# Performance work log

Measured on AMD Instinct MI355X. Metric: run time of the kernel, lower is better.

The kernel has to match this reference:

```python
import jax, jax.numpy as jnp
import numpy as np

N = 8192
NUM_CLASSES = 81            # background + 80 fg classes (COCO)
SCORE_THRESH = 0.05
NMS_THRESH = 0.5
NUM_DETECTIONS = 100
REG_W = (10.0, 10.0, 5.0, 5.0)
MIN_SIZE = 1.0
BBOX_XFORM_CLIP = float(np.log(1000.0 / 16.0))


def setup_inputs() -> dict:
    key = jax.random.key(0)
    k1, k2, k3, k4 = jax.random.split(key, 4)
    xy1 = jax.random.uniform(k1, (N, 2), minval=0.0, maxval=700.0)
    wh = jax.random.uniform(k2, (N, 2), minval=8.0, maxval=300.0)
    proposal = jnp.concatenate([xy1, xy1 + wh], axis=1)          # [N,4] xyxy
    class_logit = jax.random.normal(k3, (N, NUM_CLASSES), dtype=jnp.float32)
    box_regression = jax.random.normal(k4, (N, NUM_CLASSES * 4), dtype=jnp.float32) * 0.5
    return {"proposal": proposal, "class_logit": class_logit,
            "box_regression": box_regression, "image_h": 800, "image_w": 1216}


def _decode(deltas, boxes):
    # deltas [..., N, 4] (per-class), boxes [N, 4] xyxy; standard Fast R-CNN BoxCoder.decode
    wx, wy, ww, wh = REG_W
    widths = boxes[:, 2] - boxes[:, 0]
    heights = boxes[:, 3] - boxes[:, 1]
    cx = boxes[:, 0] + 0.5 * widths
    cy = boxes[:, 1] + 0.5 * heights
    dx = deltas[..., 0] / wx
    dy = deltas[..., 1] / wy
    dw = jnp.minimum(deltas[..., 2] / ww, BBOX_XFORM_CLIP)
    dh = jnp.minimum(deltas[..., 3] / wh, BBOX_XFORM_CLIP)
    pcx = dx * widths + cx
    pcy = dy * heights + cy
    pw = jnp.exp(dw) * widths
    ph = jnp.exp(dh) * heights
    return jnp.stack([pcx - 0.5 * pw, pcy - 0.5 * ph,
                      pcx + 0.5 * pw, pcy + 0.5 * ph], axis=-1)


def _iou_one(box, boxes):
    # IoU of one box [4] against all boxes [N,4]
    lt = jnp.maximum(box[:2], boxes[:, :2])
    rb = jnp.minimum(box[2:], boxes[:, 2:])
    whc = jnp.clip(rb - lt, 0.0)
    inter = whc[:, 0] * whc[:, 1]
    a1 = (box[2] - box[0]) * (box[3] - box[1])
    a2 = (boxes[:, 2] - boxes[:, 0]) * (boxes[:, 3] - boxes[:, 1])
    return inter / (a1 + a2 - inter + 1e-12)


def _nms_per_class(boxes, scores):
    # Sequential greedy NMS: pick highest score, suppress IoU>thresh, repeat.
    # boxes [N,4], scores [N] (already 0 where filtered). Returns top NUM_DETECTIONS.
    def step(scores_w, _):
        j = jnp.argmax(scores_w)
        s = scores_w[j]
        valid = s > 0.0
        bj = boxes[j]
        iou = _iou_one(bj, boxes)                         # [N]
        new = jnp.where(iou > NMS_THRESH, 0.0, scores_w).at[j].set(0.0)
        new = jnp.where(valid, new, scores_w)
        return new, (bj, s, valid)
    _, (sel_b, sel_s, sel_v) = jax.lax.scan(step, scores, None, length=NUM_DETECTIONS)
    return sel_b, sel_s, sel_v                            # [D,4], [D], [D]


def reference(proposal, class_logit, box_regression, image_h, image_w):
    pred_score = jax.nn.softmax(class_logit, axis=-1)     # [N, C]
    deltas = box_regression.reshape(N, NUM_CLASSES, 4)
    fg_deltas = jnp.transpose(deltas[:, 1:, :], (1, 0, 2))  # [C-1, N, 4]
    boxes = _decode(fg_deltas, proposal)                    # [C-1, N, 4]
    # clip to image (process_box)
    W = jnp.float32(image_w); H = jnp.float32(image_h)
    x1 = jnp.clip(boxes[..., 0], 0.0, W)
    y1 = jnp.clip(boxes[..., 1], 0.0, H)
    x2 = jnp.clip(boxes[..., 2], 0.0, W)
    y2 = jnp.clip(boxes[..., 3], 0.0, H)
    boxes = jnp.stack([x1, y1, x2, y2], axis=-1)            # [C-1, N, 4]
    keep_size = ((x2 - x1) >= MIN_SIZE) & ((y2 - y1) >= MIN_SIZE)
    scores = jnp.transpose(pred_score[:, 1:])               # [C-1, N]
    scores = jnp.where((scores >= SCORE_THRESH) & keep_size, scores, 0.0)
    sel_b, sel_s, sel_v = jax.vmap(_nms_per_class)(boxes, scores)  # [C-1,D,...]
    out_boxes = sel_b.reshape(-1, 4)                         # [(C-1)*D, 4]
    out_scores = sel_s.reshape(-1)
    out_labels = jnp.repeat(jnp.arange(1, NUM_CLASSES, dtype=jnp.int32), NUM_DETECTIONS)
    out_valid = sel_v.reshape(-1)
    return out_boxes, out_scores, out_labels, out_valid
```

## Files before the change

kernel.cpp:

```cpp
#include <hip/hip_runtime.h>
#include <hip/hip_bf16.h>

#define NN 8192
#define NC 81
#define FG 80
#define ND 100
#define SH 8
#define CAPS 128
#define CPADI 32
#define MAXK 384
#define KW6 6
#define KROW 9
#define BBOX_CLIP 4.135166556742356f

__global__ __launch_bounds__(256) void decode_kernel(
    const float* __restrict__ prop,
    const float* __restrict__ logit,
    const float* __restrict__ reg,
    const int* __restrict__ ih, const int* __restrict__ iw,
    int* __restrict__ counts,
    float* __restrict__ boxes0,
    float* __restrict__ cbox,
    float* __restrict__ cscore)
{
    const int n = blockIdx.x * 4 + (threadIdx.x >> 6);
    const int shard = blockIdx.x & (SH - 1);
    const int lane = threadIdx.x & 63;
    const float* lrow = logit + (long)n * NC;

    float v1 = lrow[lane];
    float v2 = (lane < NC - 64) ? lrow[64 + lane] : -1e30f;
    float m = fmaxf(v1, v2);
#pragma unroll
    for (int off = 32; off; off >>= 1) m = fmaxf(m, __shfl_xor(m, off));
    float e = expf(v1 - m) + ((lane < NC - 64) ? expf(v2 - m) : 0.0f);
#pragma unroll
    for (int off = 32; off; off >>= 1) e += __shfl_xor(e, off);

    const float W = (float)iw[0];
    const float H = (float)ih[0];
    const float4 p = *(const float4*)(prop + n * 4);
    const float pw = p.z - p.x, ph = p.w - p.y;
    const float pcx = p.x + 0.5f * pw, pcy = p.y + 0.5f * ph;

    for (int c = 1 + lane; c <= FG; c += 64) {
        float score = expf(lrow[c] - m) / e;
        const float4 d = *(const float4*)(reg + (long)n * (NC * 4) + c * 4);
        float dx = d.x / 10.0f;
        float dy = d.y / 10.0f;
        float dw = fminf(d.z / 5.0f, BBOX_CLIP);
        float dh = fminf(d.w / 5.0f, BBOX_CLIP);
        float ncx = dx * pw + pcx;
        float ncy = dy * ph + pcy;
        float nw = expf(dw) * pw;
        float nh = expf(dh) * ph;
        float bx1 = ncx - 0.5f * nw, by1 = ncy - 0.5f * nh;
        float bx2 = ncx + 0.5f * nw, by2 = ncy + 0.5f * nh;
        bx1 = fminf(fmaxf(bx1, 0.0f), W);
        by1 = fminf(fmaxf(by1, 0.0f), H);
        bx2 = fminf(fmaxf(bx2, 0.0f), W);
        by2 = fminf(fmaxf(by2, 0.0f), H);
        bool keep = ((bx2 - bx1) >= 1.0f) && ((by2 - by1) >= 1.0f);

        if (n == 0) {
            float* b0 = boxes0 + (c - 1) * 4;
            b0[0] = bx1; b0[1] = by1; b0[2] = bx2; b0[3] = by2;
        }
        if (score >= 0.05f && keep) {
            const int slot = (c - 1) * SH + shard;
            int pos = atomicAdd(&counts[slot * CPADI], 1);
            if (pos < CAPS) {
                float* cb = cbox + ((long)slot * CAPS + pos) * 4;
                cb[0] = bx1; cb[1] = by1; cb[2] = bx2; cb[3] = by2;
                cscore[slot * CAPS + pos] = score;
            }
        }
    }
}

__global__ __launch_bounds__(1024) void nms_kernel(
    const int* __restrict__ counts,
    const float* __restrict__ boxes0,
    const float* __restrict__ cbox,
    const float* __restrict__ cscore,
    float* __restrict__ out)
{
    __shared__ __align__(16) float  s_sc[MAXK];
    __shared__ float4 s_ubox[MAXK];
    __shared__ int    s_sidx[MAXK];
    __shared__ float4 s_box[MAXK];
    __shared__ float  s_ss[MAXK];
    __shared__ unsigned long long s_row[MAXK * KROW];

    const int c = blockIdx.x;
    const int t = threadIdx.x;
    const int lane = t & 63;
    const int wv = t >> 6;

    int cnt0 = min(counts[(c * SH + 0) * CPADI], CAPS);
    int cnt1 = min(counts[(c * SH + 1) * CPADI], CAPS);
    int cnt2 = min(counts[(c * SH + 2) * CPADI], CAPS);
    int cnt3 = min(counts[(c * SH + 3) * CPADI], CAPS);
    int cnt4 = min(counts[(c * SH + 4) * CPADI], CAPS);
    int cnt5 = min(counts[(c * SH + 5) * CPADI], CAPS);
    int cnt6 = min(counts[(c * SH + 6) * CPADI], CAPS);
    int cnt7 = min(counts[(c * SH + 7) * CPADI], CAPS);
    int K = cnt0 + cnt1 + cnt2 + cnt3 + cnt4 + cnt5 + cnt6 + cnt7;
    if (K > MAXK) K = MAXK;
    const int KW = (K + 63) >> 6;


    for (int i = K + t; i < MAXK; i += 1024) {
        s_sc[i] = 0.0f;
        s_ss[i] = 0.0f;
        s_box[i] = make_float4(0.f, 0.f, 0.f, 0.f);
    }
    {
        const int s = t >> 7;
        const int i = t & (CAPS - 1);
        int mycnt = cnt0;
        if (s == 1) mycnt = cnt1; if (s == 2) mycnt = cnt2;
        if (s == 3) mycnt = cnt3; if (s == 4) mycnt = cnt4;
        if (s == 5) mycnt = cnt5; if (s == 6) mycnt = cnt6;
        if (s == 7) mycnt = cnt7;
        int offs = 0;
        if (s > 0) offs += cnt0; if (s > 1) offs += cnt1;
        if (s > 2) offs += cnt2; if (s > 3) offs += cnt3;
        if (s > 4) offs += cnt4; if (s > 5) offs += cnt5;
        if (s > 6) offs += cnt6;
        if (i < mycnt) {
            int d = offs + i;
            if (d < MAXK) {
                const long src = (long)(c * SH + s) * CAPS + i;
                s_sc[d] = cscore[src];
                s_ubox[d] = *(const float4*)(cbox + src * 4);
            }
        }
    }
    __syncthreads();

    if (t < K) {
        const float si = s_sc[t];
        const float4* s4 = (const float4*)s_sc;
        const int nch = (K + 3) >> 2;
        int r = 0;
        for (int ch = 0; ch < nch; ++ch) {
            const float4 sj = s4[ch];
            const int j = ch * 4;
            r += (sj.x > si) || (sj.x == si && (j + 0) < t);
            r += (sj.y > si) || (sj.y == si && (j + 1) < t);
            r += (sj.z > si) || (sj.z == si && (j + 2) < t);
            r += (sj.w > si) || (sj.w == si && (j + 3) < t);
        }
        s_sidx[r] = t;
    }
    __syncthreads();

    if (t < K) {
        const int i = s_sidx[t];
        s_box[t] = s_ubox[i];
        s_ss[t] = s_sc[i];
    }
    __syncthreads();

    float4 colb[KW6];
    float a2c[KW6];
#pragma unroll
    for (int w = 0; w < KW6; ++w) {
        const float4 b = s_box[w * 64 + lane];
        colb[w] = b;
        a2c[w] = (b.z - b.x) * (b.w - b.y);
    }

    for (int r = wv; r < K; r += 16) {
        const float4 rb = s_box[r];
        const float a1 = (rb.z - rb.x) * (rb.w - rb.y);
#pragma unroll
        for (int w = 0; w < KW6; ++w) {
            if (w < KW) {
                const float lx = fmaxf(rb.x, colb[w].x);
                const float ly = fmaxf(rb.y, colb[w].y);
                const float rx = fminf(rb.z, colb[w].z);
                const float ry = fminf(rb.w, colb[w].w);
                const float cw = fmaxf(rx - lx, 0.0f);
                const float ch = fmaxf(ry - ly, 0.0f);
                const float inter = cw * ch;
                const float iou = inter / (a1 + a2c[w] - inter + 1e-12f);
                const unsigned long long msk = __ballot(iou > 0.5f);
                if (lane == 0) s_row[r * KROW + w] = msk;
            }
        }
    }
    __syncthreads();

    if (wv != 0) return;

#define INIW(W) ((K >= (W)*64 + 64) ? ~0ull : ((K <= (W)*64) ? 0ull : ((~0ull) >> (64 - (K - (W)*64)))))
    const unsigned long long va0 = INIW(0), va1 = INIW(1), va2 = INIW(2);
    const unsigned long long va3 = INIW(3), va4 = INIW(4), va5 = INIW(5);
#undef INIW

    const unsigned long long ltm = (1ull << lane) - 1ull;

    unsigned long long v0 = va0, v1 = va1, v2 = va2;
    unsigned long long v3 = va3, v4 = va4, v5 = va5;

    for (int it = 0; it < MAXK; ++it) {
        unsigned long long nv0, nv1, nv2, nv3, nv4, nv5;
        {
            const unsigned long long* rp = s_row + (unsigned)(0 * 64 + lane) * KROW;
            unsigned long long s = rp[0] & v0 & ltm;
            nv0 = __ballot(s == 0ull) & va0;
        }
        {
            const unsigned long long* rp = s_row + (unsigned)(1 * 64 + lane) * KROW;
            unsigned long long s = (rp[0] & v0) | (rp[1] & v1 & ltm);
            nv1 = __ballot(s == 0ull) & va1;
        }
        {
            const unsigned long long* rp = s_row + (unsigned)(2 * 64 + lane) * KROW;
            unsigned long long s = (rp[0] & v0) | (rp[1] & v1) | (rp[2] & v2 & ltm);
            nv2 = __ballot(s == 0ull) & va2;
        }
        {
            const unsigned long long* rp = s_row + (unsigned)(3 * 64 + lane) * KROW;
            unsigned long long s = (rp[0] & v0) | (rp[1] & v1) | (rp[2] & v2) |
                                   (rp[3] & v3 & ltm);
            nv3 = __ballot(s == 0ull) & va3;
        }
        {
            const unsigned long long* rp = s_row + (unsigned)(4 * 64 + lane) * KROW;
            unsigned long long s = (rp[0] & v0) | (rp[1] & v1) | (rp[2] & v2) |
                                   (rp[3] & v3) | (rp[4] & v4 & ltm);
            nv4 = __ballot(s == 0ull) & va4;
        }
        {
            const unsigned long long* rp = s_row + (unsigned)(5 * 64 + lane) * KROW;
            unsigned long long s = (rp[0] & v0) | (rp[1] & v1) | (rp[2] & v2) |
                                   (rp[3] & v3) | (rp[4] & v4) | (rp[5] & v5 & ltm);
            nv5 = __ballot(s == 0ull) & va5;
        }
        const unsigned long long diff = (nv0 ^ v0) | (nv1 ^ v1) | (nv2 ^ v2) |
                                        (nv3 ^ v3) | (nv4 ^ v4) | (nv5 ^ v5);
        v0 = nv0; v1 = nv1; v2 = nv2; v3 = nv3; v4 = nv4; v5 = nv5;
        if (diff == 0ull) break;
    }

    float* ob = out + (long)c * ND * 4;
    float* os = out + (long)FG * ND * 4 + c * ND;
    float* ol = os + FG * ND;
    float* ov = ol + FG * ND;
    const float lab = (float)(c + 1);

    const int p0 = __popcll(v0), p1 = __popcll(v1), p2 = __popcll(v2);
    const int p3 = __popcll(v3), p4 = __popcll(v4);
    const int total = p0 + p1 + p2 + p3 + p4 + __popcll(v5);
    const int kept = total < ND ? total : ND;

    const float b0x1 = boxes0[c * 4 + 0], b0y1 = boxes0[c * 4 + 1];
    const float b0x2 = boxes0[c * 4 + 2], b0y2 = boxes0[c * 4 + 3];

    for (int d = lane; d < ND; d += 64) {
        if (d < kept) {
            int rr = d;
            unsigned long long x;
            int wbase;
            if (rr < p0) { x = v0; wbase = 0; }
            else { rr -= p0;
                if (rr < p1) { x = v1; wbase = 64; }
                else { rr -= p1;
                    if (rr < p2) { x = v2; wbase = 128; }
                    else { rr -= p2;
                        if (rr < p3) { x = v3; wbase = 192; }
                        else { rr -= p3;
                            if (rr < p4) { x = v4; wbase = 256; }
                            else { rr -= p4; x = v5; wbase = 320; }
                        }
                    }
                }
            }
            for (int k = 0; k < rr; ++k) x &= x - 1ull;
            const int i_d = wbase + __builtin_ctzll(x);
            const float4 kb = s_box[i_d];
            *(float4*)(ob + d * 4) = kb;
            os[d] = s_ss[i_d]; ol[d] = lab; ov[d] = 1.0f;
        } else {
            *(float4*)(ob + d * 4) = make_float4(b0x1, b0y1, b0x2, b0y2);
            os[d] = 0.0f; ol[d] = lab; ov[d] = 0.0f;
        }
    }
}

extern "C" void kernel_launch(void* const* d_in, const int* in_sizes, int n_in,
                              void* d_out, int out_size, void* d_ws, size_t ws_size,
                              hipStream_t stream) {
    const float* prop  = (const float*)d_in[0];
    const float* logit = (const float*)d_in[1];
    const float* reg   = (const float*)d_in[2];
    const int*   ih    = (const int*)d_in[3];
    const int*   iw    = (const int*)d_in[4];
    float* out = (float*)d_out;

    char* ws = (char*)d_ws;
    int*   counts = (int*)ws;
    float* boxes0 = (float*)(ws + 81920);
    float* cscore = (float*)(ws + 90112);
    float* cbox   = (float*)(ws + 90112 + (size_t)FG * SH * CAPS * 4);

    hipMemsetAsync(counts, 0, FG * SH * CPADI * sizeof(int), stream);
    decode_kernel<<<NN / 4, 256, 0, stream>>>(prop, logit, reg, ih, iw,
                                              counts, boxes0, cbox, cscore);
    nms_kernel<<<FG, 1024, 0, stream>>>(counts, boxes0, cbox, cscore, out);
}
```

Before: 106.7 us.

## Fuse decode and NMS into one kernel with a global atomic barrier

```diff
diff --git a/kernel.cpp b/kernel.cpp
--- a/kernel.cpp
+++ b/kernel.cpp
@@ -1,5 +1,4 @@
 #include <hip/hip_runtime.h>
-#include <hip/hip_bf16.h>
 
 #define NN 8192
 #define NC 81
@@ -11,78 +10,20 @@
 #define MAXK 384
 #define KW6 6
 #define KROW 9
+#define NBLK 512
+#define PPB 16
 #define BBOX_CLIP 4.135166556742356f
 
-__global__ __launch_bounds__(256) void decode_kernel(
+__global__ __launch_bounds__(1024) void fused_kernel(
     const float* __restrict__ prop,
     const float* __restrict__ logit,
     const float* __restrict__ reg,
     const int* __restrict__ ih, const int* __restrict__ iw,
     int* __restrict__ counts,
+    int* __restrict__ done,
     float* __restrict__ boxes0,
     float* __restrict__ cbox,
-    float* __restrict__ cscore)
-{
-    const int n = blockIdx.x * 4 + (threadIdx.x >> 6);
-    const int shard = blockIdx.x & (SH - 1);
-    const int lane = threadIdx.x & 63;
-    const float* lrow = logit + (long)n * NC;
-
-    float v1 = lrow[lane];
-    float v2 = (lane < NC - 64) ? lrow[64 + lane] : -1e30f;
-    float m = fmaxf(v1, v2);
-#pragma unroll
-    for (int off = 32; off; off >>= 1) m = fmaxf(m, __shfl_xor(m, off));
-    float e = expf(v1 - m) + ((lane < NC - 64) ? expf(v2 - m) : 0.0f);
-#pragma unroll
-    for (int off = 32; off; off >>= 1) e += __shfl_xor(e, off);
-
-    const float W = (float)iw[0];
-    const float H = (float)ih[0];
-    const float4 p = *(const float4*)(prop + n * 4);
-    const float pw = p.z - p.x, ph = p.w - p.y;
-    const float pcx = p.x + 0.5f * pw, pcy = p.y + 0.5f * ph;
-
-    for (int c = 1 + lane; c <= FG; c += 64) {
-        float score = expf(lrow[c] - m) / e;
-        const float4 d = *(const float4*)(reg + (long)n * (NC * 4) + c * 4);
-        float dx = d.x / 10.0f;
-        float dy = d.y / 10.0f;
-        float dw = fminf(d.z / 5.0f, BBOX_CLIP);
-        float dh = fminf(d.w / 5.0f, BBOX_CLIP);
-        float ncx = dx * pw + pcx;
-        float ncy = dy * ph + pcy;
-        float nw = expf(dw) * pw;
-        float nh = expf(dh) * ph;
-        float bx1 = ncx - 0.5f * nw, by1 = ncy - 0.5f * nh;
-        float bx2 = ncx + 0.5f * nw, by2 = ncy + 0.5f * nh;
-        bx1 = fminf(fmaxf(bx1, 0.0f), W);
-        by1 = fminf(fmaxf(by1, 0.0f), H);
-        bx2 = fminf(fmaxf(bx2, 0.0f), W);
-        by2 = fminf(fmaxf(by2, 0.0f), H);
-        bool keep = ((bx2 - bx1) >= 1.0f) && ((by2 - by1) >= 1.0f);
-
-        if (n == 0) {
-            float* b0 = boxes0 + (c - 1) * 4;
-            b0[0] = bx1; b0[1] = by1; b0[2] = bx2; b0[3] = by2;
-        }
-        if (score >= 0.05f && keep) {
-            const int slot = (c - 1) * SH + shard;
-            int pos = atomicAdd(&counts[slot * CPADI], 1);
-            if (pos < CAPS) {
-                float* cb = cbox + ((long)slot * CAPS + pos) * 4;
-                cb[0] = bx1; cb[1] = by1; cb[2] = bx2; cb[3] = by2;
-                cscore[slot * CAPS + pos] = score;
-            }
-        }
-    }
-}
-
-__global__ __launch_bounds__(1024) void nms_kernel(
-    const int* __restrict__ counts,
-    const float* __restrict__ boxes0,
-    const float* __restrict__ cbox,
-    const float* __restrict__ cscore,
+    float* __restrict__ cscore,
     float* __restrict__ out)
 {
     __shared__ __align__(16) float  s_sc[MAXK];
@@ -92,10 +33,84 @@
     __shared__ float  s_ss[MAXK];
     __shared__ unsigned long long s_row[MAXK * KROW];
 
-    const int c = blockIdx.x;
+    const int b = blockIdx.x;
     const int t = threadIdx.x;
     const int lane = t & 63;
     const int wv = t >> 6;
+
+    {
+        const int n = b * PPB + wv;
+        const int shard = b & (SH - 1);
+        const float* lrow = logit + (long)n * NC;
+
+        float v1 = lrow[lane];
+        float v2 = (lane < NC - 64) ? lrow[64 + lane] : -1e30f;
+        float m = fmaxf(v1, v2);
+#pragma unroll
+        for (int off = 32; off; off >>= 1) m = fmaxf(m, __shfl_xor(m, off));
+        float e = expf(v1 - m) + ((lane < NC - 64) ? expf(v2 - m) : 0.0f);
+#pragma unroll
+        for (int off = 32; off; off >>= 1) e += __shfl_xor(e, off);
+
+        const float W = (float)iw[0];
+        const float H = (float)ih[0];
+        const float4 p = *(const float4*)(prop + n * 4);
+        const float pw = p.z - p.x, ph = p.w - p.y;
+        const float pcx = p.x + 0.5f * pw, pcy = p.y + 0.5f * ph;
+
+        for (int c = 1 + lane; c <= FG; c += 64) {
+            float score = expf(lrow[c] - m) / e;
+            const float4 d = *(const float4*)(reg + (long)n * (NC * 4) + c * 4);
+            float dx = d.x / 10.0f;
+            float dy = d.y / 10.0f;
+            float dw = fminf(d.z / 5.0f, BBOX_CLIP);
+            float dh = fminf(d.w / 5.0f, BBOX_CLIP);
+            float ncx = dx * pw + pcx;
+            float ncy = dy * ph + pcy;
+            float nw = expf(dw) * pw;
+            float nh = expf(dh) * ph;
+            float bx1 = ncx - 0.5f * nw, by1 = ncy - 0.5f * nh;
+            float bx2 = ncx + 0.5f * nw, by2 = ncy + 0.5f * nh;
+            bx1 = fminf(fmaxf(bx1, 0.0f), W);
+            by1 = fminf(fmaxf(by1, 0.0f), H);
+            bx2 = fminf(fmaxf(bx2, 0.0f), W);
+            by2 = fminf(fmaxf(by2, 0.0f), H);
+            bool keep = ((bx2 - bx1) >= 1.0f) && ((by2 - by1) >= 1.0f);
+
+            if (n == 0) {
+                float* b0 = boxes0 + (c - 1) * 4;
+                b0[0] = bx1; b0[1] = by1; b0[2] = bx2; b0[3] = by2;
+            }
+            if (score >= 0.05f && keep) {
+                const int slot = (c - 1) * SH + shard;
+                int pos = atomicAdd(&counts[slot * CPADI], 1);
+                if (pos < CAPS) {
+                    float* cb = cbox + ((long)slot * CAPS + pos) * 4;
+                    cb[0] = bx1; cb[1] = by1; cb[2] = bx2; cb[3] = by2;
+                    cscore[slot * CAPS + pos] = score;
+                }
+            }
+        }
+    }
+
+    __threadfence();
+    __syncthreads();
+    if (t == 0) {
+        __hip_atomic_fetch_add(done, 1, __ATOMIC_RELEASE,
+                               __HIP_MEMORY_SCOPE_AGENT);
+    }
+    if (b >= FG) return;
+
+    if (t == 0) {
+        while (__hip_atomic_load(done, __ATOMIC_ACQUIRE,
+                                 __HIP_MEMORY_SCOPE_AGENT) < NBLK) {
+            __builtin_amdgcn_s_sleep(2);
+        }
+    }
+    __syncthreads();
+    __threadfence();
+
+    const int c = b;
 
     int cnt0 = min(counts[(c * SH + 0) * CPADI], CAPS);
     int cnt1 = min(counts[(c * SH + 1) * CPADI], CAPS);
@@ -108,7 +123,6 @@
     int K = cnt0 + cnt1 + cnt2 + cnt3 + cnt4 + cnt5 + cnt6 + cnt7;
     if (K > MAXK) K = MAXK;
     const int KW = (K + 63) >> 6;
-
 
     for (int i = K + t; i < MAXK; i += 1024) {
         s_sc[i] = 0.0f;
@@ -167,9 +181,9 @@
     float a2c[KW6];
 #pragma unroll
     for (int w = 0; w < KW6; ++w) {
-        const float4 b = s_box[w * 64 + lane];
-        colb[w] = b;
-        a2c[w] = (b.z - b.x) * (b.w - b.y);
+        const float4 bb = s_box[w * 64 + lane];
+        colb[w] = bb;
+        a2c[w] = (bb.z - bb.x) * (bb.w - bb.y);
     }
 
     for (int r = wv; r < K; r += 16) {
@@ -303,12 +317,13 @@
 
     char* ws = (char*)d_ws;
     int*   counts = (int*)ws;
-    float* boxes0 = (float*)(ws + 81920);
+    int*   done   = (int*)(ws + 81920);
+    float* boxes0 = (float*)(ws + 82048);
     float* cscore = (float*)(ws + 90112);
     float* cbox   = (float*)(ws + 90112 + (size_t)FG * SH * CAPS * 4);
 
-    hipMemsetAsync(counts, 0, FG * SH * CPADI * sizeof(int), stream);
-    decode_kernel<<<NN / 4, 256, 0, stream>>>(prop, logit, reg, ih, iw,
-                                              counts, boxes0, cbox, cscore);
-    nms_kernel<<<FG, 1024, 0, stream>>>(counts, boxes0, cbox, cscore, out);
+    hipMemsetAsync(ws, 0, 82048, stream);
+    fused_kernel<<<NBLK, 1024, 0, stream>>>(prop, logit, reg, ih, iw,
+                                            counts, done, boxes0, cbox, cscore,
+                                            out);
 }
```

Measured after the change: 284.3 us. 2.66x slower.

## Replace atomic sharded candidate buckets with dense transposed score array and in-NMS compaction

Applied to the files above, without the earlier changes.

```diff
diff --git a/kernel.cpp b/kernel.cpp
--- a/kernel.cpp
+++ b/kernel.cpp
@@ -1,13 +1,9 @@
 #include <hip/hip_runtime.h>
-#include <hip/hip_bf16.h>
 
 #define NN 8192
 #define NC 81
 #define FG 80
 #define ND 100
-#define SH 8
-#define CAPS 128
-#define CPADI 32
 #define MAXK 384
 #define KW6 6
 #define KROW 9
@@ -18,13 +14,11 @@
     const float* __restrict__ logit,
     const float* __restrict__ reg,
     const int* __restrict__ ih, const int* __restrict__ iw,
-    int* __restrict__ counts,
     float* __restrict__ boxes0,
-    float* __restrict__ cbox,
-    float* __restrict__ cscore)
+    float* __restrict__ cscoreT,
+    float* __restrict__ cboxT)
 {
     const int n = blockIdx.x * 4 + (threadIdx.x >> 6);
-    const int shard = blockIdx.x & (SH - 1);
     const int lane = threadIdx.x & 63;
     const float* lrow = logit + (long)n * NC;
 
@@ -61,81 +55,75 @@
         bx2 = fminf(fmaxf(bx2, 0.0f), W);
         by2 = fminf(fmaxf(by2, 0.0f), H);
         bool keep = ((bx2 - bx1) >= 1.0f) && ((by2 - by1) >= 1.0f);
+        bool pass = (score >= 0.05f) && keep;
 
         if (n == 0) {
             float* b0 = boxes0 + (c - 1) * 4;
             b0[0] = bx1; b0[1] = by1; b0[2] = bx2; b0[3] = by2;
         }
-        if (score >= 0.05f && keep) {
-            const int slot = (c - 1) * SH + shard;
-            int pos = atomicAdd(&counts[slot * CPADI], 1);
-            if (pos < CAPS) {
-                float* cb = cbox + ((long)slot * CAPS + pos) * 4;
-                cb[0] = bx1; cb[1] = by1; cb[2] = bx2; cb[3] = by2;
-                cscore[slot * CAPS + pos] = score;
-            }
+        const long o = (long)(c - 1) * NN + n;
+        cscoreT[o] = pass ? score : 0.0f;
+        if (pass) {
+            *(float4*)(cboxT + o * 4) = make_float4(bx1, by1, bx2, by2);
         }
     }
 }
 
 __global__ __launch_bounds__(1024) void nms_kernel(
-    const int* __restrict__ counts,
     const float* __restrict__ boxes0,
-    const float* __restrict__ cbox,
-    const float* __restrict__ cscore,
+    const float* __restrict__ cscoreT,
+    const float* __restrict__ cboxT,
     float* __restrict__ out)
 {
     __shared__ __align__(16) float  s_sc[MAXK];
+    __shared__ int    s_n[MAXK];
     __shared__ float4 s_ubox[MAXK];
     __shared__ int    s_sidx[MAXK];
     __shared__ float4 s_box[MAXK];
     __shared__ float  s_ss[MAXK];
     __shared__ unsigned long long s_row[MAXK * KROW];
-
-    const int c = blockIdx.x;
+    __shared__ int    s_cnt;
+
+    const int c0 = blockIdx.x;
     const int t = threadIdx.x;
     const int lane = t & 63;
     const int wv = t >> 6;
-
-    int cnt0 = min(counts[(c * SH + 0) * CPADI], CAPS);
-    int cnt1 = min(counts[(c * SH + 1) * CPADI], CAPS);
-    int cnt2 = min(counts[(c * SH + 2) * CPADI], CAPS);
-    int cnt3 = min(counts[(c * SH + 3) * CPADI], CAPS);
-    int cnt4 = min(counts[(c * SH + 4) * CPADI], CAPS);
-    int cnt5 = min(counts[(c * SH + 5) * CPADI], CAPS);
-    int cnt6 = min(counts[(c * SH + 6) * CPADI], CAPS);
-    int cnt7 = min(counts[(c * SH + 7) * CPADI], CAPS);
-    int K = cnt0 + cnt1 + cnt2 + cnt3 + cnt4 + cnt5 + cnt6 + cnt7;
+    const unsigned long long ltm = (1ull << lane) - 1ull;
+
+    if (t == 0) s_cnt = 0;
+    __syncthreads();
+
+    const float* srow = cscoreT + (long)c0 * NN;
+    for (int base = 0; base < NN; base += 1024) {
+        const int n = base + t;
+        const float s = srow[n];
+        const bool pred = s > 0.0f;
+        const unsigned long long mask = __ballot(pred);
+        const int cnt = __popcll(mask);
+        const int prefix = __popcll(mask & ltm);
+        int wbase = 0;
+        if (lane == 0 && cnt) wbase = atomicAdd(&s_cnt, cnt);
+        wbase = __shfl(wbase, 0);
+        const int d = wbase + prefix;
+        if (pred && d < MAXK) {
+            s_sc[d] = s;
+            s_n[d] = n;
+        }
+    }
+    __syncthreads();
+
+    int K = s_cnt;
     if (K > MAXK) K = MAXK;
     const int KW = (K + 63) >> 6;
-
 
     for (int i = K + t; i < MAXK; i += 1024) {
         s_sc[i] = 0.0f;
         s_ss[i] = 0.0f;
         s_box[i] = make_float4(0.f, 0.f, 0.f, 0.f);
     }
-    {
-        const int s = t >> 7;
-        const int i = t & (CAPS - 1);
-        int mycnt = cnt0;
-        if (s == 1) mycnt = cnt1; if (s == 2) mycnt = cnt2;
-        if (s == 3) mycnt = cnt3; if (s == 4) mycnt = cnt4;
-        if (s == 5) mycnt = cnt5; if (s == 6) mycnt = cnt6;
-        if (s == 7) mycnt = cnt7;
-        int offs = 0;
-        if (s > 0) offs += cnt0; if (s > 1) offs += cnt1;
-        if (s > 2) offs += cnt2; if (s > 3) offs += cnt3;
-        if (s > 4) offs += cnt4; if (s > 5) offs += cnt5;
-        if (s > 6) offs += cnt6;
-        if (i < mycnt) {
-            int d = offs + i;
-            if (d < MAXK) {
-                const long src = (long)(c * SH + s) * CAPS + i;
-                s_sc[d] = cscore[src];
-                s_ubox[d] = *(const float4*)(cbox + src * 4);
-            }
-        }
+    if (t < K) {
+        const long o = (long)c0 * NN + s_n[t];
+        s_ubox[t] = *(const float4*)(cboxT + o * 4);
     }
     __syncthreads();
 
@@ -167,9 +155,9 @@
     float a2c[KW6];
 #pragma unroll
     for (int w = 0; w < KW6; ++w) {
-        const float4 b = s_box[w * 64 + lane];
-        colb[w] = b;
-        a2c[w] = (b.z - b.x) * (b.w - b.y);
+        const float4 bb = s_box[w * 64 + lane];
+        colb[w] = bb;
+        a2c[w] = (bb.z - bb.x) * (bb.w - bb.y);
     }
 
     for (int r = wv; r < K; r += 16) {
@@ -200,8 +188,6 @@
     const unsigned long long va3 = INIW(3), va4 = INIW(4), va5 = INIW(5);
 #undef INIW
 
-    const unsigned long long ltm = (1ull << lane) - 1ull;
-
     unsigned long long v0 = va0, v1 = va1, v2 = va2;
     unsigned long long v3 = va3, v4 = va4, v5 = va5;
 
@@ -246,19 +232,19 @@
         if (diff == 0ull) break;
     }
 
-    float* ob = out + (long)c * ND * 4;
-    float* os = out + (long)FG * ND * 4 + c * ND;
+    float* ob = out + (long)c0 * ND * 4;
+    float* os = out + (long)FG * ND * 4 + c0 * ND;
     float* ol = os + FG * ND;
     float* ov = ol + FG * ND;
-    const float lab = (float)(c + 1);
+    const float lab = (float)(c0 + 1);
 
     const int p0 = __popcll(v0), p1 = __popcll(v1), p2 = __popcll(v2);
     const int p3 = __popcll(v3), p4 = __popcll(v4);
     const int total = p0 + p1 + p2 + p3 + p4 + __popcll(v5);
     const int kept = total < ND ? total : ND;
 
-    const float b0x1 = boxes0[c * 4 + 0], b0y1 = boxes0[c * 4 + 1];
-    const float b0x2 = boxes0[c * 4 + 2], b0y2 = boxes0[c * 4 + 3];
+    const float b0x1 = boxes0[c0 * 4 + 0], b0y1 = boxes0[c0 * 4 + 1];
+    const float b0x2 = boxes0[c0 * 4 + 2], b0y2 = boxes0[c0 * 4 + 3];
 
     for (int d = lane; d < ND; d += 64) {
         if (d < kept) {
@@ -302,13 +288,11 @@
     float* out = (float*)d_out;
 
     char* ws = (char*)d_ws;
-    int*   counts = (int*)ws;
-    float* boxes0 = (float*)(ws + 81920);
-    float* cscore = (float*)(ws + 90112);
-    float* cbox   = (float*)(ws + 90112 + (size_t)FG * SH * CAPS * 4);
-
-    hipMemsetAsync(counts, 0, FG * SH * CPADI * sizeof(int), stream);
+    float* boxes0  = (float*)ws;
+    float* cscoreT = (float*)(ws + 4096);
+    float* cboxT   = (float*)(ws + 4096 + (size_t)FG * NN * 4);
+
     decode_kernel<<<NN / 4, 256, 0, stream>>>(prop, logit, reg, ih, iw,
-                                              counts, boxes0, cbox, cscore);
-    nms_kernel<<<FG, 1024, 0, stream>>>(counts, boxes0, cbox, cscore, out);
+                                              boxes0, cscoreT, cboxT);
+    nms_kernel<<<FG, 1024, 0, stream>>>(boxes0, cscoreT, cboxT, out);
 }
```

Result: no change. 108.4 us (+1.6%).
